# Kernel tuning notes

Measured on AMD Instinct MI355X. Metric: run time of the kernel, lower is better.

## Reference

```python
import jax, jax.numpy as jnp
import numpy as np

NUM_HEADS = 8
GROUPS = 32
EPS = 1e-5


def group_norm(x, gamma, beta):
    # x: [B, C, H, W], normalize over (C/G, H, W) per group
    B, C, H, W = x.shape
    xg = x.reshape(B, GROUPS, -1)
    mu = xg.mean(axis=-1, keepdims=True)
    var = xg.var(axis=-1, keepdims=True)
    xg = (xg - mu) * jax.lax.rsqrt(var + EPS)
    x = xg.reshape(B, C, H, W)
    return x * gamma[None, :, None, None] + beta[None, :, None, None]


def reference(x, w_qkv, w_out, b_out, temperature, g1, beta1, g2, beta2,
              w_mlp1, b_mlp1, w_mlp2, b_mlp2):
    B, C, H, W = x.shape
    hd = C // NUM_HEADS
    N = H * W
    identity = x

    xn = group_norm(x, g1, beta1)
    # 1x1 conv == per-pixel matmul
    qkv = jnp.einsum('oc,bchw->bohw', w_qkv, xn)  # [B, 3C, H, W]
    q, k, v = jnp.split(qkv, 3, axis=1)
    q = q.reshape(B, NUM_HEADS, hd, N)
    k = k.reshape(B, NUM_HEADS, hd, N)
    v = v.reshape(B, NUM_HEADS, hd, N)

    temp = jnp.clip(temperature, 1e-4, 10.0)  # [heads,1,1]
    attn = jnp.einsum('bhdi,bhdj->bhij', q, k) * temp[None]  # [B,h,N,N]
    attn = jax.nn.softmax(attn, axis=-1)  # max-subtract is folded into stable softmax

    out = jnp.einsum('bhdj,bhij->bhdi', v, attn)  # [B,h,hd,N]
    out = out.reshape(B, C, H, W)
    out = jnp.einsum('oc,bchw->bohw', w_out, out) + b_out[None, :, None, None]
    x = identity + out

    y = group_norm(x, g2, beta2)
    h = jnp.einsum('oc,bchw->bohw', w_mlp1, y) + b_mlp1[None, :, None, None]
    h = jax.nn.gelu(h, approximate=False)
    m = jnp.einsum('oc,bchw->bohw', w_mlp2, h) + b_mlp2[None, :, None, None]
    return x + m


def setup_inputs() -> dict:
    key = jax.random.key(0)
    ks = jax.random.split(key, 8)
    C = 256
    B, H, W = 2, 64, 64
    hid = C // 4
    s_in = 1.0 / np.sqrt(C)
    s_hid = 1.0 / np.sqrt(hid)
    return {
        'x': jax.random.normal(ks[0], (B, C, H, W), jnp.float32),
        'w_qkv': jax.random.normal(ks[1], (3 * C, C), jnp.float32) * s_in,
        'w_out': jax.random.normal(ks[2], (C, C), jnp.float32) * s_in,
        'b_out': jnp.zeros((C,), jnp.float32),
        'temperature': jnp.ones((NUM_HEADS, 1, 1), jnp.float32) * (C // NUM_HEADS) ** -0.5,
        'g1': jnp.ones((C,), jnp.float32),
        'beta1': jnp.zeros((C,), jnp.float32),
        'g2': jnp.ones((C,), jnp.float32),
        'beta2': jnp.zeros((C,), jnp.float32),
        'w_mlp1': jax.random.normal(ks[3], (hid, C), jnp.float32) * s_in,
        'b_mlp1': jnp.zeros((hid,), jnp.float32),
        'w_mlp2': jax.random.normal(ks[4], (C, hid), jnp.float32) * s_hid,
        'b_mlp2': jnp.zeros((C,), jnp.float32),
    }
```

## Files before the change

### kernel.cpp

```cpp
#include <hip/hip_runtime.h>
#include <hip/hip_bf16.h>
#include <math.h>

#define NB 2
#define NC 256
#define NHEAD 8
#define HD 32
#define NPIX 4096
#define GEPS 1e-5f
#define NCHUNK 2
#define JLEN (NPIX / NCHUNK)

typedef short bf16x8 __attribute__((ext_vector_type(8)));
typedef float f32x4 __attribute__((ext_vector_type(4)));

typedef __attribute__((address_space(3))) unsigned int lds_u32;
typedef __attribute__((address_space(1))) const unsigned int glb_u32;

union U16x8 { uint4 u4; uint2 u2[2]; unsigned u32[4]; unsigned short us[8]; bf16x8 v; };

__device__ inline unsigned short tobf(float f) {
  union { float f; unsigned u; } c; c.f = f;
  return (unsigned short)((c.u + 0x7FFFu + ((c.u >> 16) & 1u)) >> 16);
}
__device__ inline unsigned packtrunc(float lo, float hi) {
  return __builtin_amdgcn_perm(__float_as_uint(hi), __float_as_uint(lo), 0x07060302u);
}
__device__ inline float geluf(float v) {
  return 0.5f * v * (1.f + erff(v * 0.70710678118654752f));
}

__device__ inline int detect_bf(const void* xraw) {
  __shared__ int flg;
  int t = threadIdx.x;
  if (t < 64) {
    unsigned short h = ((const unsigned short*)xraw)[2 * t];
    unsigned e = (h >> 7) & 0xFFu;
    int weird = (e < 113u || e > 140u) ? 1 : 0;
    unsigned long long m = __ballot(weird);
    if (t == 0) flg = (__popcll(m) > 16) ? 0 : 1;
  }
  __syncthreads();
  return flg;
}

struct ConvArgs { const void* src[13]; int off[14]; };

__device__ inline float ldsrc(const void* p, int idx, int bf) {
  if (bf) {
    unsigned v = ((const unsigned short*)p)[idx];
    return __uint_as_float(v << 16);
  }
  return ((const float*)p)[idx];
}

__global__ __launch_bounds__(256) void conv_prep_kernel(
    ConvArgs a, float* __restrict__ dstbase, int total,
    unsigned short* __restrict__ wqkv_b, unsigned short* __restrict__ wout_b,
    unsigned short* __restrict__ wm1_b, unsigned short* __restrict__ wm2_b,
    float* __restrict__ qscale, float* __restrict__ part1p) {
  int bf = detect_bf(a.src[0]);
  int blk = blockIdx.x, t = threadIdx.x;
  int i = blk * 256 + t;
  float val = 0.f;
  if (i < total) {
    int s = 0;
    while (i >= a.off[s + 1]) ++s;
    val = ldsrc(a.src[s], i - a.off[s], bf);
    dstbase[i] = val;
  }
  if (blk < 8192) {
    __shared__ float rs[256], rq[256];
    rs[t] = val;
    rq[t] = val * val;
    __syncthreads();
    for (int o = 128; o > 0; o >>= 1) {
      if (t < o) { rs[t] += rs[t + o]; rq[t] += rq[t + o]; }
      __syncthreads();
    }
    if (t == 0) { part1p[blk * 2] = rs[0]; part1p[blk * 2 + 1] = rq[0]; }
  }
  if (i < 196608) wqkv_b[i] = tobf(ldsrc(a.src[1], i, bf));
  else if (i < 262144) wout_b[i - 196608] = tobf(ldsrc(a.src[2], i - 196608, bf));
  else if (i < 278528) wm1_b[i - 262144] = tobf(ldsrc(a.src[9], i - 262144, bf));
  else if (i < 294912) wm2_b[i - 278528] = tobf(ldsrc(a.src[11], i - 278528, bf));
  if (i < 768) {
    if (i < 256) {
      float tc = fminf(fmaxf(ldsrc(a.src[4], i >> 5, bf), 1e-4f), 10.f);
      qscale[i] = tc * 1.4426950408889634f;
    } else qscale[i] = 1.0f;
  }
}

__global__ __launch_bounds__(256) void qkv_fused_kernel(
    const float* __restrict__ x_f, const float* __restrict__ part1p,
    const float* __restrict__ g1, const float* __restrict__ be1,
    const unsigned short* __restrict__ W, const float* __restrict__ qscale,
    unsigned short* __restrict__ qn, unsigned short* __restrict__ kn,
    unsigned short* __restrict__ vs) {
  int t = threadIdx.x;
  int w = t >> 6, lane = t & 63, l16 = lane & 15, quad = lane >> 4;
  int p0 = blockIdx.x * 16;
  int b = p0 >> 12;
  __shared__ float red[32][8][2];
  __shared__ float sm[32], si[32];
  {
    int g = t >> 3, seg = t & 7;
    float s = 0.f, s2 = 0.f;
    const float* pp = part1p + ((size_t)(b * 32 + g) * 128 + seg * 16) * 2;
#pragma unroll
    for (int k = 0; k < 16; ++k) { s += pp[k * 2]; s2 += pp[k * 2 + 1]; }
    red[g][seg][0] = s; red[g][seg][1] = s2;
  }
  __syncthreads();
  if (t < 32) {
    float s = 0.f, s2 = 0.f;
#pragma unroll
    for (int k = 0; k < 8; ++k) { s += red[t][k][0]; s2 += red[t][k][1]; }
    float mean = s * (1.f / 32768.f);
    float var = s2 * (1.f / 32768.f) - mean * mean;
    sm[t] = mean; si[t] = rsqrtf(var + GEPS);
  }
  __syncthreads();
  __shared__ unsigned short Ys[16][264];
  {
    int p = t & 15, cg = t >> 4;
    int n = (p0 & 4095) + p;
    const float* src = x_f + ((size_t)b * NC + cg * 16) * NPIX + n;
    U16x8 lo, hi;
#pragma unroll
    for (int cc = 0; cc < 16; ++cc) {
      int c = cg * 16 + cc;
      int g = c >> 3;
      float gg = g1[c] * si[g];
      float vv = (src[(size_t)cc * NPIX] - sm[g]) * gg + be1[c];
      if (cc < 8) lo.us[cc] = tobf(vv); else hi.us[cc - 8] = tobf(vv);
    }
    *(uint4*)&Ys[p][cg * 16] = lo.u4;
    *(uint4*)&Ys[p][cg * 16 + 8] = hi.u4;
  }
  __syncthreads();
  int ob = blockIdx.y * 384 + w * 96;
  f32x4 acc[6] = {};
#pragma unroll
  for (int k0 = 0; k0 < 256; k0 += 32) {
    U16x8 bfr; bfr.u4 = *(const uint4*)&Ys[l16][k0 + quad * 8];
#pragma unroll
    for (int ot = 0; ot < 6; ++ot) {
      U16x8 af;
      af.u4 = *(const uint4*)(W + (size_t)(ob + ot * 16 + l16) * 256 + k0 + quad * 8);
      acc[ot] = __builtin_amdgcn_mfma_f32_16x16x32_bf16(af.v, bfr.v, acc[ot], 0, 0, 0);
    }
  }
  int n = (p0 & 4095) + l16;
#pragma unroll
  for (int ot = 0; ot < 6; ++ot) {
    int oc = ob + ot * 16 + quad * 4;
    float v[4];
#pragma unroll
    for (int r = 0; r < 4; ++r) v[r] = acc[ot][r] * qscale[oc + r];
    int sec = oc >> 8;
    int c = oc & 255;
    if (sec < 2) {
      int hh = c >> 5, d = c & 31;
      unsigned short* base = sec == 0 ? qn : kn;
      uint2 pk;
      pk.x = (unsigned)tobf(v[0]) | ((unsigned)tobf(v[1]) << 16);
      pk.y = (unsigned)tobf(v[2]) | ((unsigned)tobf(v[3]) << 16);
      *(uint2*)(base + ((size_t)(b * NHEAD + hh) * NPIX + n) * HD + d) = pk;
    } else {
#pragma unroll
      for (int r = 0; r < 4; ++r)
        vs[((size_t)(b * NC + c + r)) * NPIX + n] = tobf(v[r]);
    }
  }
}

__global__ __launch_bounds__(512) void attn9_kernel(
    const unsigned short* __restrict__ qn, const unsigned short* __restrict__ kn,
    const unsigned short* __restrict__ vs, float* __restrict__ pO,
    float* __restrict__ pl) {
  int bx = blockIdx.x;
  int iblk = bx & 31, chunk = bx >> 5;
  int i0 = iblk * 128;
  int jbase = chunk * JLEN;
  int h = blockIdx.y, b = blockIdx.z;
  int bh = b * NHEAD + h;
  int t = threadIdx.x;
  int w = t >> 6, lane = t & 63, l16 = lane & 15, quad = lane >> 4;

  __shared__ unsigned short Kt[2048];
  __shared__ unsigned short Vt[2048];
  __shared__ unsigned short Pl[8][16][72];

  U16x8 qf;
  qf.u4 = *(const uint4*)(qn + ((size_t)bh * NPIX + i0 + w * 16 + l16) * HD + quad * 8);
  U16x8 ones;
#pragma unroll
  for (int j = 0; j < 8; ++j) ones.us[j] = 0x3F80;

  const unsigned short* gp;
  lds_u32* dst;
  if (w < 4) {
    int kj = (w << 4) + (lane >> 2);
    int kg = (lane & 3) ^ ((kj >> 1) & 3);
    gp = kn + ((size_t)bh * NPIX + jbase + kj) * HD + kg * 8;
    dst = (lds_u32*)&Kt[w * 512];
  } else {
    int vd = ((w - 4) << 3) + (lane >> 3);
    int vg = (lane & 7) ^ (vd & 7);
    gp = vs + ((size_t)(b * NC + h * HD + vd)) * NPIX + jbase + vg * 8;
    dst = (lds_u32*)&Vt[(w - 4) * 512];
  }
  int gstep = (w < 4) ? 64 * HD : 64;

  f32x4 o0 = {0.f, 0.f, 0.f, 0.f}, o1 = {0.f, 0.f, 0.f, 0.f};
  f32x4 lacc = {0.f, 0.f, 0.f, 0.f};
  const f32x4 zf = {0.f, 0.f, 0.f, 0.f};

  int sp = (quad ^ ((l16 >> 1) & 3)) * 8;
  for (int jt = 0; jt < JLEN; jt += 64) {
    __builtin_amdgcn_global_load_lds((glb_u32*)gp, dst, 16, 0, 0);
    gp += gstep;
    __syncthreads();
    f32x4 st[4];
#pragma unroll
    for (int jj = 0; jj < 4; ++jj) {
      U16x8 kf; kf.u4 = *(const uint4*)&Kt[(jj * 16 + l16) * 32 + sp];
      st[jj] = __builtin_amdgcn_mfma_f32_16x16x32_bf16(kf.v, qf.v, zf, 0, 0, 0);
    }
#pragma unroll
    for (int jj = 0; jj < 4; ++jj) {
      uint2 pk;
      pk.x = packtrunc(__builtin_amdgcn_exp2f(st[jj][0]), __builtin_amdgcn_exp2f(st[jj][1]));
      pk.y = packtrunc(__builtin_amdgcn_exp2f(st[jj][2]), __builtin_amdgcn_exp2f(st[jj][3]));
      *(uint2*)&Pl[w][l16][jj * 16 + quad * 4] = pk;
    }
#pragma unroll
    for (int ks = 0; ks < 2; ++ks) {
      U16x8 pb; pb.u4 = *(const uint4*)&Pl[w][l16][ks * 32 + quad * 8];
      int vp = ((ks * 4 + quad) ^ (l16 & 7)) * 8;
      U16x8 va; va.u4 = *(const uint4*)&Vt[l16 * 64 + vp];
      U16x8 vb2; vb2.u4 = *(const uint4*)&Vt[(16 + l16) * 64 + vp];
      o0 = __builtin_amdgcn_mfma_f32_16x16x32_bf16(va.v, pb.v, o0, 0, 0, 0);
      o1 = __builtin_amdgcn_mfma_f32_16x16x32_bf16(vb2.v, pb.v, o1, 0, 0, 0);
      lacc = __builtin_amdgcn_mfma_f32_16x16x32_bf16(ones.v, pb.v, lacc, 0, 0, 0);
    }
    __syncthreads();
  }

  int pr = bh * 64 + iblk * 2 + (w >> 2);
  float* ob = pO + ((size_t)chunk * 1024 + pr) * 2048;
  int icol = (w & 3) * 16 + l16;
#pragma unroll
  for (int r = 0; r < 4; ++r) {
    ob[(quad * 4 + r) * 64 + icol] = o0[r];
    ob[(16 + quad * 4 + r) * 64 + icol] = o1[r];
  }
  if (quad == 0)
    pl[((size_t)chunk * 1024 + pr) * 64 + icol] = lacc[0];
}

__global__ __launch_bounds__(256) void wout_kernel(
    const unsigned short* __restrict__ W, const float* __restrict__ pO,
    const float* __restrict__ pl, const float* __restrict__ bias,
    const float* __restrict__ res, float* __restrict__ xres_t,
    float* __restrict__ part2p) {
  int t = threadIdx.x;
  int w = t >> 6, lane = t & 63, l16 = lane & 15, quad = lane >> 4;
  int p = blockIdx.x * 16 + l16;
  int b = p >> 12, n = p & 4095;
  int i = p & 63, iblk = (p >> 6) & 63;
  int ob = w * 64;
  float rinv8[8];
#pragma unroll
  for (int hh = 0; hh < 8; ++hh) {
    size_t pr = (size_t)(b * NHEAD + hh) * 64 + iblk;
    float l = pl[pr * 64 + i] + pl[(1024 + pr) * 64 + i];
    rinv8[hh] = 1.f / l;
  }
  f32x4 acc[4] = {};
#pragma unroll
  for (int k0 = 0; k0 < 256; k0 += 32) {
    int hh = k0 >> 5;
    const float* q0 = pO + ((size_t)(b * NHEAD + hh) * 64 + iblk) * 2048 + quad * 8 * 64 + i;
    const float* q1 = q0 + (size_t)1024 * 2048;
    float rv = rinv8[hh];
    U16x8 bfr;
#pragma unroll
    for (int u = 0; u < 4; ++u) {
      float va = (q0[(2 * u) * 64] + q1[(2 * u) * 64]) * rv;
      float vb = (q0[(2 * u + 1) * 64] + q1[(2 * u + 1) * 64]) * rv;
      bfr.u32[u] = packtrunc(va, vb);
    }
#pragma unroll
    for (int ot = 0; ot < 4; ++ot) {
      U16x8 af;
      af.u4 = *(const uint4*)(W + (size_t)(ob + ot * 16 + l16) * 256 + k0 + quad * 8);
      acc[ot] = __builtin_amdgcn_mfma_f32_16x16x32_bf16(af.v, bfr.v, acc[ot], 0, 0, 0);
    }
  }
  __shared__ float sb[256][4][2];
#pragma unroll
  for (int ot = 0; ot < 4; ++ot) {
    int oc = ob + ot * 16 + quad * 4;
    float s = 0.f, s2 = 0.f;
    float v4[4];
#pragma unroll
    for (int r = 0; r < 4; ++r) {
      float vv = acc[ot][r] + bias[oc + r] + res[((size_t)(b * NC + oc + r)) * NPIX + n];
      v4[r] = vv;
      s += vv; s2 += vv * vv;
    }
    *(float4*)&xres_t[(size_t)p * NC + oc] = make_float4(v4[0], v4[1], v4[2], v4[3]);
    sb[t][ot][0] = s; sb[t][ot][1] = s2;
  }
  __syncthreads();
  if (t < 32) {
    int ww = t >> 3, rem = t & 7, ot = rem >> 1, qp = rem & 1;
    float s = 0.f, s2 = 0.f;
#pragma unroll
    for (int q = 2 * qp; q < 2 * qp + 2; ++q)
      for (int l = 0; l < 16; ++l) {
        int tt = ww * 64 + q * 16 + l;
        s += sb[tt][ot][0]; s2 += sb[tt][ot][1];
      }
    size_t idx = ((size_t)(b * 32 + t) * 256 + (blockIdx.x & 255)) * 2;
    part2p[idx] = s; part2p[idx + 1] = s2;
  }
}

__global__ __launch_bounds__(256) void mlp_fused_kernel(
    const void* __restrict__ xraw, const float* __restrict__ xres_t,
    const float* __restrict__ part2p, const float* __restrict__ g2,
    const float* __restrict__ be2, const unsigned short* __restrict__ W1,
    const float* __restrict__ b1, const unsigned short* __restrict__ W2,
    const float* __restrict__ b2, void* __restrict__ dout) {
  int wbf = detect_bf(xraw);
  int t = threadIdx.x;
  int w = t >> 6, lane = t & 63, l16 = lane & 15, quad = lane >> 4;
  int p0 = blockIdx.x * 16;
  int b = p0 >> 12;
  __shared__ float red[32][8][2];
  __shared__ float sm[32], si[32];
  {
    int g = t >> 3, seg = t & 7;
    float s = 0.f, s2 = 0.f;
    const float* pp = part2p + ((size_t)(b * 32 + g) * 256 + seg * 32) * 2;
#pragma unroll
    for (int k = 0; k < 32; ++k) { s += pp[k * 2]; s2 += pp[k * 2 + 1]; }
    red[g][seg][0] = s; red[g][seg][1] = s2;
  }
  __syncthreads();
  if (t < 32) {
    float s = 0.f, s2 = 0.f;
#pragma unroll
    for (int k = 0; k < 8; ++k) { s += red[t][k][0]; s2 += red[t][k][1]; }
    float mean = s * (1.f / 32768.f);
    float var = s2 * (1.f / 32768.f) - mean * mean;
    sm[t] = mean; si[t] = rsqrtf(var + GEPS);
  }
  __syncthreads();
  __shared__ float Xs[16][261];
  __shared__ unsigned short Ys[16][264];
  {
    int p = t >> 4, cg = t & 15;
    const float* src = xres_t + (size_t)(p0 + p) * NC + cg * 16;
    U16x8 lo, hi;
#pragma unroll
    for (int cc = 0; cc < 16; ++cc) {
      int c = cg * 16 + cc;
      int g = c >> 3;
      float v = src[cc];
      Xs[p][c] = v;
      float yv = (v - sm[g]) * (g2[c] * si[g]) + be2[c];
      if (cc < 8) lo.us[cc] = tobf(yv); else hi.us[cc - 8] = tobf(yv);
    }
    *(uint4*)&Ys[p][cg * 16] = lo.u4;
    *(uint4*)&Ys[p][cg * 16 + 8] = hi.u4;
  }
  __syncthreads();
  f32x4 a1 = {0.f, 0.f, 0.f, 0.f};
#pragma unroll
  for (int k0 = 0; k0 < 256; k0 += 32) {
    U16x8 bfr; bfr.u4 = *(const uint4*)&Ys[l16][k0 + quad * 8];
    U16x8 af;
    af.u4 = *(const uint4*)(W1 + (size_t)(w * 16 + l16) * 256 + k0 + quad * 8);
    a1 = __builtin_amdgcn_mfma_f32_16x16x32_bf16(af.v, bfr.v, a1, 0, 0, 0);
  }
  __shared__ unsigned short Hs[16][72];
  {
    int oc = w * 16 + quad * 4;
    float h0 = geluf(a1[0] + b1[oc]),     h1 = geluf(a1[1] + b1[oc + 1]);
    float h2 = geluf(a1[2] + b1[oc + 2]), h3 = geluf(a1[3] + b1[oc + 3]);
    uint2 pk;
    pk.x = (unsigned)tobf(h0) | ((unsigned)tobf(h1) << 16);
    pk.y = (unsigned)tobf(h2) | ((unsigned)tobf(h3) << 16);
    *(uint2*)&Hs[l16][oc] = pk;
  }
  __syncthreads();
  f32x4 a2[4] = {};
#pragma unroll
  for (int k0 = 0; k0 < 64; k0 += 32) {
    U16x8 bfr; bfr.u4 = *(const uint4*)&Hs[l16][k0 + quad * 8];
#pragma unroll
    for (int ot = 0; ot < 4; ++ot) {
      U16x8 af;
      af.u4 = *(const uint4*)(W2 + (size_t)(w * 64 + ot * 16 + l16) * 64 + k0 + quad * 8);
      a2[ot] = __builtin_amdgcn_mfma_f32_16x16x32_bf16(af.v, bfr.v, a2[ot], 0, 0, 0);
    }
  }
  int n = (p0 & 4095) + l16;
#pragma unroll
  for (int ot = 0; ot < 4; ++ot) {
    int oc = w * 64 + ot * 16 + quad * 4;
#pragma unroll
    for (int r = 0; r < 4; ++r) {
      float v = a2[ot][r] + b2[oc + r] + Xs[l16][oc + r];
      size_t oidx = ((size_t)(b * NC + oc + r)) * NPIX + n;
      if (wbf) ((__hip_bfloat16*)dout)[oidx] = __float2bfloat16(v);
      else ((float*)dout)[oidx] = v;
    }
  }
}

extern "C" void kernel_launch(void* const* d_in, const int* in_sizes, int n_in,
                              void* d_out, int out_size, void* d_ws, size_t ws_size,
                              hipStream_t stream) {
  float* ws = (float*)d_ws;
  size_t off = 16;
  float* x_f    = ws + off; off += (size_t)NB * NC * NPIX;
  float* wqkv_f = ws + off; off += 768 * 256;
  float* wout_f = ws + off; off += 256 * 256;
  float* bout_f = ws + off; off += 256;
  float* temp_f = ws + off; off += 8;
  float* g1_f   = ws + off; off += 256;
  float* be1_f  = ws + off; off += 256;
  float* g2_f   = ws + off; off += 256;
  float* be2_f  = ws + off; off += 256;
  float* wm1_f  = ws + off; off += 64 * 256;
  float* bm1_f  = ws + off; off += 64;
  float* wm2_f  = ws + off; off += 256 * 64;
  float* bm2_f  = ws + off; off += 256;
  float* xres   = ws + off; off += (size_t)NB * NC * NPIX;
  unsigned short* qn     = (unsigned short*)(ws + off); off += 1048576;
  unsigned short* kn     = (unsigned short*)(ws + off); off += 1048576;
  unsigned short* vs     = (unsigned short*)(ws + off); off += 1048576;
  unsigned short* wqkv_b = (unsigned short*)(ws + off); off += 98304;
  unsigned short* wout_b = (unsigned short*)(ws + off); off += 32768;
  unsigned short* wm1_b  = (unsigned short*)(ws + off); off += 8192;
  unsigned short* wm2_b  = (unsigned short*)(ws + off); off += 8192;
  float* qscale = ws + off; off += 768;
  float* part1p = ws + off; off += 16384;
  float* part2p = ws + off; off += 65536;
  float* pO     = ws + off; off += (size_t)NCHUNK * 1024 * 2048;
  float* plb    = ws + off; off += (size_t)NCHUNK * 1024 * 64;
  (void)wqkv_f; (void)wout_f; (void)wm1_f; (void)wm2_f; (void)temp_f; (void)bm1_f;

  ConvArgs ca;
  int acc = 0;
  for (int i = 0; i < 13; ++i) {
    ca.src[i] = d_in[i];
    ca.off[i] = acc;
    acc += (i < n_in) ? in_sizes[i] : 0;
  }
  ca.off[13] = acc;
  conv_prep_kernel<<<(acc + 255) / 256, 256, 0, stream>>>(
      ca, x_f, acc, wqkv_b, wout_b, wm1_b, wm2_b, qscale, part1p);

  qkv_fused_kernel<<<dim3(512, 2), 256, 0, stream>>>(
      x_f, part1p, g1_f, be1_f, wqkv_b, qscale, qn, kn, vs);

  attn9_kernel<<<dim3(32 * NCHUNK, NHEAD, NB), 512, 0, stream>>>(qn, kn, vs, pO, plb);

  wout_kernel<<<512, 256, 0, stream>>>(wout_b, pO, plb, bout_f, x_f, xres, part2p);

  mlp_fused_kernel<<<512, 256, 0, stream>>>(
      d_in[0], xres, part2p, g2_f, be2_f, wm1_b, bm1_f, wm2_b, bm2_f, d_out);
}
```

Baseline: 214.9 us.

## Double-buffer K/V tiles in attention with async prefetch and XCD-aware block mapping

Attention kernel now double-buffers the K and V LDS tiles, issuing the next tile's global-to-LDS load before computing the current one. It replaces the two __syncthreads per tile with explicit vmcnt waits and raw barriers, and raises wave priority around the MFMA sections. It also flattens the grid into a 1D launch whose block index is remapped so that blocks sharing the same (b,h,chunk) K/V data land on the same XCD, improving L2 reuse. The cost is more LDS and a hand-scheduled loop that assumes exactly 32 tiles per chunk.

```diff
diff --git a/kernel.cpp b/kernel.cpp
--- a/kernel.cpp
+++ b/kernel.cpp
@@ -176,21 +176,25 @@
   }
 }
 
-__global__ __launch_bounds__(512) void attn9_kernel(
+__global__ __launch_bounds__(512) void attn10_kernel(
     const unsigned short* __restrict__ qn, const unsigned short* __restrict__ kn,
     const unsigned short* __restrict__ vs, float* __restrict__ pO,
     float* __restrict__ pl) {
-  int bx = blockIdx.x;
-  int iblk = bx & 31, chunk = bx >> 5;
+  int f = blockIdx.x;
+  int xcd = f & 7, slot = f >> 3;
+  int s = xcd + ((slot >> 5) << 3);
+  int iblk = slot & 31;
+  int chunk = s & 1;
+  int h = (s >> 1) & 7;
+  int b = s >> 4;
   int i0 = iblk * 128;
   int jbase = chunk * JLEN;
-  int h = blockIdx.y, b = blockIdx.z;
   int bh = b * NHEAD + h;
   int t = threadIdx.x;
   int w = t >> 6, lane = t & 63, l16 = lane & 15, quad = lane >> 4;
 
-  __shared__ unsigned short Kt[2048];
-  __shared__ unsigned short Vt[2048];
+  __shared__ unsigned short Kt[2][2048];
+  __shared__ unsigned short Vt[2][2048];
   __shared__ unsigned short Pl[8][16][72];
 
   U16x8 qf;
@@ -200,17 +204,19 @@
   for (int j = 0; j < 8; ++j) ones.us[j] = 0x3F80;
 
   const unsigned short* gp;
-  lds_u32* dst;
+  lds_u32* dstN[2];
   if (w < 4) {
     int kj = (w << 4) + (lane >> 2);
     int kg = (lane & 3) ^ ((kj >> 1) & 3);
     gp = kn + ((size_t)bh * NPIX + jbase + kj) * HD + kg * 8;
-    dst = (lds_u32*)&Kt[w * 512];
+    dstN[0] = (lds_u32*)&Kt[0][w * 512];
+    dstN[1] = (lds_u32*)&Kt[1][w * 512];
   } else {
     int vd = ((w - 4) << 3) + (lane >> 3);
     int vg = (lane & 7) ^ (vd & 7);
     gp = vs + ((size_t)(b * NC + h * HD + vd)) * NPIX + jbase + vg * 8;
-    dst = (lds_u32*)&Vt[(w - 4) * 512];
+    dstN[0] = (lds_u32*)&Vt[0][(w - 4) * 512];
+    dstN[1] = (lds_u32*)&Vt[1][(w - 4) * 512];
   }
   int gstep = (w < 4) ? 64 * HD : 64;
 
@@ -219,35 +225,60 @@
   const f32x4 zf = {0.f, 0.f, 0.f, 0.f};
 
   int sp = (quad ^ ((l16 >> 1) & 3)) * 8;
-  for (int jt = 0; jt < JLEN; jt += 64) {
-    __builtin_amdgcn_global_load_lds((glb_u32*)gp, dst, 16, 0, 0);
-    gp += gstep;
-    __syncthreads();
-    f32x4 st[4];
-#pragma unroll
-    for (int jj = 0; jj < 4; ++jj) {
-      U16x8 kf; kf.u4 = *(const uint4*)&Kt[(jj * 16 + l16) * 32 + sp];
-      st[jj] = __builtin_amdgcn_mfma_f32_16x16x32_bf16(kf.v, qf.v, zf, 0, 0, 0);
-    }
-#pragma unroll
-    for (int jj = 0; jj < 4; ++jj) {
-      uint2 pk;
-      pk.x = packtrunc(__builtin_amdgcn_exp2f(st[jj][0]), __builtin_amdgcn_exp2f(st[jj][1]));
-      pk.y = packtrunc(__builtin_amdgcn_exp2f(st[jj][2]), __builtin_amdgcn_exp2f(st[jj][3]));
-      *(uint2*)&Pl[w][l16][jj * 16 + quad * 4] = pk;
-    }
-#pragma unroll
-    for (int ks = 0; ks < 2; ++ks) {
-      U16x8 pb; pb.u4 = *(const uint4*)&Pl[w][l16][ks * 32 + quad * 8];
-      int vp = ((ks * 4 + quad) ^ (l16 & 7)) * 8;
-      U16x8 va; va.u4 = *(const uint4*)&Vt[l16 * 64 + vp];
-      U16x8 vb2; vb2.u4 = *(const uint4*)&Vt[(16 + l16) * 64 + vp];
-      o0 = __builtin_amdgcn_mfma_f32_16x16x32_bf16(va.v, pb.v, o0, 0, 0, 0);
-      o1 = __builtin_amdgcn_mfma_f32_16x16x32_bf16(vb2.v, pb.v, o1, 0, 0, 0);
-      lacc = __builtin_amdgcn_mfma_f32_16x16x32_bf16(ones.v, pb.v, lacc, 0, 0, 0);
-    }
-    __syncthreads();
-  }
+
+  __builtin_amdgcn_global_load_lds((glb_u32*)gp, dstN[0], 16, 0, 0);
+  gp += gstep;
+
+#define ATTN_STEP(CUR, VMC, ISSUE)                                              \
+  {                                                                             \
+    if (ISSUE) {                                                                \
+      __builtin_amdgcn_global_load_lds((glb_u32*)gp, dstN[(CUR) ^ 1], 16, 0, 0);\
+      gp += gstep;                                                              \
+    }                                                                           \
+    asm volatile("s_waitcnt vmcnt(" #VMC ")" ::: "memory");                     \
+    __builtin_amdgcn_s_barrier();                                               \
+    __builtin_amdgcn_sched_barrier(0);                                          \
+    f32x4 st[4];                                                                \
+    __builtin_amdgcn_s_setprio(1);                                              \
+    _Pragma("unroll")                                                           \
+    for (int jj = 0; jj < 4; ++jj) {                                            \
+      U16x8 kf; kf.u4 = *(const uint4*)&Kt[CUR][(jj * 16 + l16) * 32 + sp];     \
+      st[jj] = __builtin_amdgcn_mfma_f32_16x16x32_bf16(kf.v, qf.v, zf, 0, 0, 0);\
+    }                                                                           \
+    __builtin_amdgcn_s_setprio(0);                                              \
+    _Pragma("unroll")                                                           \
+    for (int jj = 0; jj < 4; ++jj) {                                            \
+      uint2 pk;                                                                 \
+      pk.x = packtrunc(__builtin_amdgcn_exp2f(st[jj][0]),                       \
+                       __builtin_amdgcn_exp2f(st[jj][1]));                      \
+      pk.y = packtrunc(__builtin_amdgcn_exp2f(st[jj][2]),                       \
+                       __builtin_amdgcn_exp2f(st[jj][3]));                      \
+      *(uint2*)&Pl[w][l16][jj * 16 + quad * 4] = pk;                            \
+    }                                                                           \
+    __builtin_amdgcn_s_setprio(1);                                              \
+    _Pragma("unroll")                                                           \
+    for (int ks = 0; ks < 2; ++ks) {                                            \
+      U16x8 pb; pb.u4 = *(const uint4*)&Pl[w][l16][ks * 32 + quad * 8];         \
+      int vp = ((ks * 4 + quad) ^ (l16 & 7)) * 8;                               \
+      U16x8 va; va.u4 = *(const uint4*)&Vt[CUR][l16 * 64 + vp];                 \
+      U16x8 vb2; vb2.u4 = *(const uint4*)&Vt[CUR][(16 + l16) * 64 + vp];        \
+      o0 = __builtin_amdgcn_mfma_f32_16x16x32_bf16(va.v, pb.v, o0, 0, 0, 0);    \
+      o1 = __builtin_amdgcn_mfma_f32_16x16x32_bf16(vb2.v, pb.v, o1, 0, 0, 0);   \
+      lacc = __builtin_amdgcn_mfma_f32_16x16x32_bf16(ones.v, pb.v, lacc, 0, 0, 0);\
+    }                                                                           \
+    __builtin_amdgcn_s_setprio(0);                                              \
+    __builtin_amdgcn_sched_barrier(0);                                          \
+    __builtin_amdgcn_s_barrier();                                               \
+  }
+
+#pragma unroll 1
+  for (int it = 0; it < 15; ++it) {
+    ATTN_STEP(0, 1, 1)
+    ATTN_STEP(1, 1, 1)
+  }
+  ATTN_STEP(0, 1, 1)
+  ATTN_STEP(1, 0, 0)
+#undef ATTN_STEP
 
   int pr = bh * 64 + iblk * 2 + (w >> 2);
   float* ob = pO + ((size_t)chunk * 1024 + pr) * 2048;
@@ -471,7 +502,7 @@
   qkv_fused_kernel<<<dim3(512, 2), 256, 0, stream>>>(
       x_f, part1p, g1_f, be1_f, wqkv_b, qscale, qn, kn, vs);
 
-  attn9_kernel<<<dim3(32 * NCHUNK, NHEAD, NB), 512, 0, stream>>>(qn, kn, vs, pO, plb);
+  attn10_kernel<<<dim3(1024), 512, 0, stream>>>(qn, kn, vs, pO, plb);
 
   wout_kernel<<<512, 256, 0, stream>>>(wout_b, pO, plb, bout_f, x_f, xres, part2p);
 
```

New measurement: 208.5 us. 3.0% less time.
